# Kernel tuning notes

Hardware: AMD Instinct MI355X
Metric: run time of the kernel (lower is better)

The kernel has to match this reference:

```python
import jax, jax.numpy as jnp
import numpy as np

DIM = 768
NUM_HEADS = 12
HEAD_DIM = DIM // NUM_HEADS
SCALE = HEAD_DIM ** -0.5
NEG = -9e15


def setup_inputs() -> dict:
    key = jax.random.key(0)
    ks = jax.random.split(key, 8)
    B, N, M, C = 4, 1024, 2048, DIM
    q = jax.random.normal(ks[0], (B, N, C), dtype=jnp.float32)
    kv = jax.random.normal(ks[1], (B, M, C), dtype=jnp.float32)
    mask = jax.random.randint(ks[2], (B, 1, N, M), 0, 2, dtype=jnp.int32)
    s = 1.0 / np.sqrt(C)
    Wq = jax.random.normal(ks[3], (C, C), dtype=jnp.float32) * s      # nn.Linear(dim, dim), no bias
    Wkv = jax.random.normal(ks[4], (2 * C, C), dtype=jnp.float32) * s  # nn.Linear(dim, 2*dim), no bias
    Wproj = jax.random.normal(ks[5], (C, C), dtype=jnp.float32) * s
    bproj = jax.random.normal(ks[6], (C,), dtype=jnp.float32) * s
    return {"q": q, "kv": kv, "Wq": Wq, "Wkv": Wkv, "Wproj": Wproj, "bproj": bproj, "mask": mask}


def reference(q, kv, Wq, Wkv, Wproj, bproj, mask):
    B, M, C = kv.shape
    _, N, _ = q.shape
    H, d = NUM_HEADS, HEAD_DIM
    # kv projection -> [B, M, 2, H, d] -> k, v: [B, H, M, d]
    kvp = (kv @ Wkv.T).reshape(B, M, 2, H, d)
    k = kvp[:, :, 0].transpose(0, 2, 1, 3)
    v = kvp[:, :, 1].transpose(0, 2, 1, 3)
    # q projection -> [B, H, N, d], pre-scaled
    qp = (q @ Wq.T).reshape(B, N, H, d).transpose(0, 2, 1, 3) * SCALE
    attn = jnp.einsum('bhnd,bhmd->bhnm', qp, k)  # [B, H, N, M]
    attn = jnp.where(mask == 0, NEG, attn)
    attn = jax.nn.softmax(attn, axis=-1)
    # attn_drop / proj_drop have rate 0.0 (eval): identity
    x = jnp.einsum('bhnm,bhmd->bhnd', attn, v)
    x = x.transpose(0, 2, 1, 3).reshape(B, N, C)
    x = x @ Wproj.T + bproj
    return x
```

## Files before the change

kernel.cpp:

```cpp
#include <hip/hip_runtime.h>
#include <hip/hip_bf16.h>


typedef short    s16x8  __attribute__((ext_vector_type(8)));
typedef short    s16x4  __attribute__((ext_vector_type(4)));
typedef __bf16   bf16x8 __attribute__((ext_vector_type(8)));
typedef float    f32x4  __attribute__((ext_vector_type(4)));
typedef _Float16 f16x4  __attribute__((ext_vector_type(4)));
typedef _Float16 f16x2  __attribute__((ext_vector_type(2)));

#define NUM_H 12
#define DIM   768
#define NQ    1024
#define MK    2048
#define QK_SCALE_LOG2E 0.18033688f

__device__ __forceinline__ short f2b(float v) {
    __hip_bfloat16 h = __float2bfloat16(v);
    return __builtin_bit_cast(short, h);
}
__device__ __forceinline__ short f2h(float v) {
    _Float16 h = (_Float16)v;
    return __builtin_bit_cast(short, h);
}
__device__ __forceinline__ f32x4 mfma_bf16_k32(bf16x8 a, bf16x8 b, f32x4 c) {
    return __builtin_amdgcn_mfma_f32_16x16x32_bf16(a, b, c, 0, 0, 0);
}
__device__ __forceinline__ f32x4 mfma_f16_k16(f16x4 a, f16x4 b, f32x4 c) {
    return __builtin_amdgcn_mfma_f32_16x16x16f16(a, b, c, 0, 0, 0);
}
__device__ __forceinline__ f16x2 pk2h(float a, float b) {
    return __builtin_bit_cast(f16x2, __builtin_amdgcn_cvt_pkrtz(a, b));
}

__global__ __launch_bounds__(256) void prep_kernel(
    const float* __restrict__ q, const float* __restrict__ kv,
    const float* __restrict__ Wq, const float* __restrict__ Wkv,
    const float* __restrict__ Wp, const int* __restrict__ mask,
    short* __restrict__ q_bf, short* __restrict__ kv_bf,
    short* __restrict__ Wq_bf, short* __restrict__ Wkv_bf,
    short* __restrict__ Wp_bf, unsigned char* __restrict__ mbytes)
{
    int bid = blockIdx.x;
    if (bid < 5760) {
        const float* s; short* d; long base;
        if (bid < 1536)      { s = q;   d = q_bf;   base = (long)bid * 2048; }
        else if (bid < 4608) { s = kv;  d = kv_bf;  base = (long)(bid - 1536) * 2048; }
        else if (bid < 4896) { s = Wq;  d = Wq_bf;  base = (long)(bid - 4608) * 2048; }
        else if (bid < 5472) { s = Wkv; d = Wkv_bf; base = (long)(bid - 4896) * 2048; }
        else                 { s = Wp;  d = Wp_bf;  base = (long)(bid - 5472) * 2048; }
        long i = base + threadIdx.x * 8;
        float4 a = *(const float4*)(s + i);
        float4 b = *(const float4*)(s + i + 4);
        s16x8 r;
        r[0] = f2b(a.x); r[1] = f2b(a.y); r[2] = f2b(a.z); r[3] = f2b(a.w);
        r[4] = f2b(b.x); r[5] = f2b(b.y); r[6] = f2b(b.z); r[7] = f2b(b.w);
        *(s16x8*)(d + i) = r;
    } else {
        long base = (long)(bid - 5760) * 2048 + threadIdx.x * 8;
        int4 m0 = *(const int4*)(mask + base);
        int4 m1 = *(const int4*)(mask + base + 4);
        unsigned v = (unsigned)(m0.x != 0)        | ((unsigned)(m0.y != 0) << 1)
                   | ((unsigned)(m0.z != 0) << 2) | ((unsigned)(m0.w != 0) << 3)
                   | ((unsigned)(m1.x != 0) << 4) | ((unsigned)(m1.y != 0) << 5)
                   | ((unsigned)(m1.z != 0) << 6) | ((unsigned)(m1.w != 0) << 7);
        mbytes[base >> 3] = (unsigned char)v;
    }
}

__device__ __forceinline__ void gemm_core(
    short* smem,
    const short* __restrict__ A, const short* __restrict__ Bt,
    int Ncols, int mode, const float* __restrict__ bias,
    short* __restrict__ outb, short* __restrict__ outb2,
    float* __restrict__ outf, int bid)
{
    short (*As)[72] = (short(*)[72])smem;
    short (*Bs)[72] = (short(*)[72])(smem + 9216);

    int ntiles = Ncols >> 7;
    int m0 = (bid / ntiles) << 7;
    int n0 = (bid % ntiles) << 7;
    int t = threadIdx.x;
    int w = t >> 6, lane = t & 63, quad = lane >> 4, l16 = lane & 15;
    int wm = (w & 1) << 6, wn = (w >> 1) << 6;

    f32x4 zero4 = {0.f, 0.f, 0.f, 0.f};
    f32x4 acc[4][4];
    for (int i = 0; i < 4; i++)
        for (int j = 0; j < 4; j++) acc[i][j] = zero4;

    int lr = t >> 1;
    int lc = (t & 1) << 5;
    const short* Ap = A + (long)(m0 + lr) * DIM + lc;
    const short* Bp = Bt + (long)(n0 + lr) * DIM + lc;

    s16x8 a8[4], b8[4];
    #pragma unroll
    for (int c = 0; c < 4; c++) {
        a8[c] = *(const s16x8*)(Ap + c * 8);
        b8[c] = *(const s16x8*)(Bp + c * 8);
    }

    for (int kt = 0; kt < DIM; kt += 64) {
        __syncthreads();
        #pragma unroll
        for (int c = 0; c < 4; c++) {
            *(s16x8*)&As[lr][lc + c * 8] = a8[c];
            *(s16x8*)&Bs[lr][lc + c * 8] = b8[c];
        }
        __syncthreads();
        if (kt + 64 < DIM) {
            #pragma unroll
            for (int c = 0; c < 4; c++) {
                a8[c] = *(const s16x8*)(Ap + kt + 64 + c * 8);
                b8[c] = *(const s16x8*)(Bp + kt + 64 + c * 8);
            }
        }
        #pragma unroll
        for (int kh = 0; kh < 2; kh++) {
            bf16x8 af[4], bfr[4];
            #pragma unroll
            for (int i = 0; i < 4; i++) {
                s16x8 tmp = *(const s16x8*)&As[wm + i * 16 + l16][kh * 32 + quad * 8];
                af[i] = __builtin_bit_cast(bf16x8, tmp);
            }
            #pragma unroll
            for (int j = 0; j < 4; j++) {
                s16x8 tmp = *(const s16x8*)&Bs[wn + j * 16 + l16][kh * 32 + quad * 8];
                bfr[j] = __builtin_bit_cast(bf16x8, tmp);
            }
            #pragma unroll
            for (int i = 0; i < 4; i++)
                #pragma unroll
                for (int j = 0; j < 4; j++)
                    acc[i][j] = mfma_bf16_k32(af[i], bfr[j], acc[i][j]);
        }
    }

    __syncthreads();

    if (mode == 2) {
        #pragma unroll
        for (int i = 0; i < 4; i++)
            #pragma unroll
            for (int j = 0; j < 4; j++)
                #pragma unroll
                for (int r = 0; r < 4; r++) {
                    int row = m0 + wm + i * 16 + quad * 4 + r;
                    int col = n0 + wn + j * 16 + l16;
                    outf[(long)row * DIM + col] = acc[i][j][r] + bias[col];
                }
        return;
    }

    short (*Cs)[136] = (short(*)[136])smem;
    bool vreg = (mode == 1) && (n0 >= DIM);

    if (!vreg) {
        float sc = (mode == 0) ? QK_SCALE_LOG2E : 1.0f;
        #pragma unroll
        for (int i = 0; i < 4; i++)
            #pragma unroll
            for (int j = 0; j < 4; j++)
                #pragma unroll
                for (int r = 0; r < 4; r++)
                    Cs[wm + i * 16 + quad * 4 + r][wn + j * 16 + l16] =
                        f2b(acc[i][j][r] * sc);
    } else {
        #pragma unroll
        for (int i = 0; i < 4; i++)
            #pragma unroll
            for (int j = 0; j < 4; j++) {
                int c = wn + j * 16 + l16;
                int r0 = wm + i * 16 + quad * 4;
                s16x4 pk;
                pk[0] = f2h(acc[i][j][0]); pk[1] = f2h(acc[i][j][1]);
                pk[2] = f2h(acc[i][j][2]); pk[3] = f2h(acc[i][j][3]);
                *(s16x4*)&Cs[c][r0] = pk;
            }
    }
    __syncthreads();

    if (!vreg) {
        int hb2 = n0 >> 6;
        long rowsN = (mode == 0) ? NQ : MK;
        int b = (int)(m0 / rowsN);
        int rb = (int)(m0 % rowsN);
        short* ob0 = outb + ((long)(b * NUM_H + hb2) * rowsN + rb) * 64;
        short* ob1 = outb + ((long)(b * NUM_H + hb2 + 1) * rowsN + rb) * 64;
        #pragma unroll
        for (int k2 = 0; k2 < 8; k2++) {
            int ch = k2 * 256 + t;
            int half = ch >> 10, off = ch & 1023;
            s16x8 vd = *(const s16x8*)&Cs[off >> 3][(half << 6) + ((off & 7) << 3)];
            *(s16x8*)((half ? ob1 : ob0) + off * 8) = vd;
        }
    } else {
        int hb2 = (n0 - DIM) >> 6;
        int b = m0 >> 11, rb = m0 & 2047;
        #pragma unroll
        for (int k2 = 0; k2 < 8; k2++) {
            int ch = k2 * 256 + t;
            int c = ch >> 4, woff = (ch & 15) << 3;
            s16x8 vd = *(const s16x8*)&Cs[c][woff];
            int half = c >> 6, dd = c & 63;
            *(s16x8*)(outb2 + (((long)(b * NUM_H + hb2 + half) * 64 + dd) * MK + rb) + woff) = vd;
        }
    }
}

__global__ __launch_bounds__(256) void gemm12_kernel(
    const short* __restrict__ qbf, const short* __restrict__ Wqbf,
    const short* __restrict__ kvbf, const short* __restrict__ Wkvbf,
    short* __restrict__ qp, short* __restrict__ kk, short* __restrict__ vt)
{
    __shared__ short smem[18432];
    if (blockIdx.x < 192)
        gemm_core(smem, qbf, Wqbf, 768, 0, nullptr, qp, nullptr, nullptr, blockIdx.x);
    else
        gemm_core(smem, kvbf, Wkvbf, 1536, 1, nullptr, kk, vt, nullptr, blockIdx.x - 192);
}

__global__ __launch_bounds__(256) void gemm3_kernel(
    const short* __restrict__ xb, const short* __restrict__ Wpbf,
    const float* __restrict__ bias, float* __restrict__ out)
{
    __shared__ short smem[18432];
    gemm_core(smem, xb, Wpbf, 768, 2, bias, nullptr, nullptr, out, blockIdx.x);
}

__global__ __launch_bounds__(256) void attn_kernel(
    const short* __restrict__ qp, const short* __restrict__ kk,
    const short* __restrict__ vt, const unsigned* __restrict__ mb,
    short* __restrict__ xb)
{
    __shared__ short qs[64][72];
    __shared__ short ks[64][72];
    __shared__ short vs[64][72];

    int bid = blockIdx.x;
    int bh = bid % 48;
    int nt = bid / 48;
    int h = bh % NUM_H, b = bh / NUM_H;
    int n0 = nt << 6;
    int t = threadIdx.x, w = t >> 6, lane = t & 63, quad = lane >> 4, l16 = lane & 15;

    const short* qbase = qp + ((long)bh * NQ + n0) * 64;
    const short* kbase = kk + (long)bh * MK * 64;
    const short* vbase = vt + (long)bh * 64 * MK;
    const unsigned* mrow = mb + ((long)b * NQ + n0 + (w << 4) + l16) * 64;

    {
        int qr = t >> 2, c0 = (t & 3) << 4;
        *(s16x8*)&qs[qr][c0]     = *(const s16x8*)(qbase + qr * 64 + c0);
        *(s16x8*)&qs[qr][c0 + 8] = *(const s16x8*)(qbase + qr * 64 + c0 + 8);
    }
    __syncthreads();
    bf16x8 bq[2];
    {
        s16x8 t0 = *(const s16x8*)&qs[(w << 4) + l16][quad * 8];
        s16x8 t1 = *(const s16x8*)&qs[(w << 4) + l16][32 + quad * 8];
        bq[0] = __builtin_bit_cast(bf16x8, t0);
        bq[1] = __builtin_bit_cast(bf16x8, t1);
    }

    int sr = t >> 2, c0 = (t & 3) << 4;
    const short* kp = kbase + (long)sr * 64 + c0;
    const short* vp = vbase + (long)sr * MK + c0;

    s16x8 k0 = *(const s16x8*)(kp);
    s16x8 k1 = *(const s16x8*)(kp + 8);
    s16x8 v0 = *(const s16x8*)(vp);
    s16x8 v1 = *(const s16x8*)(vp + 8);
    uint2 mwv = *(const uint2*)(mrow);

    f32x4 zero4 = {0.f, 0.f, 0.f, 0.f};
    f32x4 o[4], ol = zero4;
    for (int j = 0; j < 4; j++) o[j] = zero4;
    const f16x4 ones = {(_Float16)1.f, (_Float16)1.f, (_Float16)1.f, (_Float16)1.f};

    for (int mt = 0; mt < MK; mt += 64) {
        __syncthreads();
        *(s16x8*)&ks[sr][c0]     = k0;
        *(s16x8*)&ks[sr][c0 + 8] = k1;
        *(s16x8*)&vs[sr][c0]     = v0;
        *(s16x8*)&vs[sr][c0 + 8] = v1;
        unsigned cm0 = mwv.x, cm1 = mwv.y;
        __syncthreads();
        if (mt + 64 < MK) {
            k0 = *(const s16x8*)(kp + (long)(mt + 64) * 64);
            k1 = *(const s16x8*)(kp + (long)(mt + 64) * 64 + 8);
            v0 = *(const s16x8*)(vp + mt + 64);
            v1 = *(const s16x8*)(vp + mt + 64 + 8);
            mwv = *(const uint2*)(mrow + ((mt + 64) >> 5));
        }

        f32x4 s[4];
        for (int j = 0; j < 4; j++) s[j] = zero4;
        #pragma unroll
        for (int kh = 0; kh < 2; kh++)
            #pragma unroll
            for (int j = 0; j < 4; j++) {
                s16x8 tk = *(const s16x8*)&ks[j * 16 + l16][kh * 32 + quad * 8];
                s[j] = mfma_bf16_k32(__builtin_bit_cast(bf16x8, tk), bq[kh], s[j]);
            }

        f16x4 pa[4];
        #pragma unroll
        for (int j = 0; j < 4; j++) {
            unsigned wsel = (j < 2) ? cm0 : cm1;
            unsigned bits = wsel >> (((j & 1) << 4) + (quad << 2));
            float p0 = (bits & 1u)        ? __builtin_amdgcn_exp2f(s[j][0]) : 0.f;
            float p1 = ((bits >> 1) & 1u) ? __builtin_amdgcn_exp2f(s[j][1]) : 0.f;
            float p2 = ((bits >> 2) & 1u) ? __builtin_amdgcn_exp2f(s[j][2]) : 0.f;
            float p3 = ((bits >> 3) & 1u) ? __builtin_amdgcn_exp2f(s[j][3]) : 0.f;
            f16x2 lo = pk2h(p0, p1);
            f16x2 hi = pk2h(p2, p3);
            pa[j] = __builtin_shufflevector(lo, hi, 0, 1, 2, 3);
        }

        #pragma unroll
        for (int j = 0; j < 4; j++) {
            ol = mfma_f16_k16(pa[j], ones, ol);
            #pragma unroll
            for (int jd = 0; jd < 4; jd++) {
                f16x4 bv = *(const f16x4*)&vs[jd * 16 + l16][j * 16 + quad * 4];
                o[jd] = mfma_f16_k16(pa[j], bv, o[jd]);
            }
        }
    }

    float linv[4];
    #pragma unroll
    for (int rr = 0; rr < 4; rr++) linv[rr] = 1.0f / ol[rr];
    short (*ps)[72] = (short(*)[72])&qs[w << 4];
    #pragma unroll
    for (int jd = 0; jd < 4; jd++)
        #pragma unroll
        for (int rr = 0; rr < 4; rr++)
            ps[quad * 4 + rr][jd * 16 + l16] = f2b(o[jd][rr] * linv[rr]);

    #pragma unroll
    for (int k2 = 0; k2 < 2; k2++) {
        int row = (lane >> 3) + k2 * 8;
        int cc = (lane & 7) << 3;
        s16x8 vd = *(const s16x8*)&ps[row][cc];
        *(s16x8*)(xb + ((long)b * NQ + n0 + (w << 4) + row) * DIM + h * 64 + cc) = vd;
    }
}

extern "C" void kernel_launch(void* const* d_in, const int* in_sizes, int n_in,
                              void* d_out, int out_size, void* d_ws, size_t ws_size,
                              hipStream_t stream)
{
    const float* q     = (const float*)d_in[0];
    const float* kv    = (const float*)d_in[1];
    const float* Wq    = (const float*)d_in[2];
    const float* Wkv   = (const float*)d_in[3];
    const float* Wproj = (const float*)d_in[4];
    const float* bproj = (const float*)d_in[5];
    const int*   mask  = (const int*)d_in[6];
    float* out = (float*)d_out;

    char* ws = (char*)d_ws;
    short* q_bf   = (short*)ws; ws += (size_t)4096 * 768 * 2;
    short* kv_bf  = (short*)ws; ws += (size_t)8192 * 768 * 2;
    short* Wq_bf  = (short*)ws; ws += (size_t)768 * 768 * 2;
    short* Wkv_bf = (short*)ws; ws += (size_t)1536 * 768 * 2;
    short* Wp_bf  = (short*)ws; ws += (size_t)768 * 768 * 2;
    short* qp     = (short*)ws; ws += (size_t)4096 * 768 * 2;
    short* kk     = (short*)ws; ws += (size_t)8192 * 768 * 2;
    short* vt     = (short*)ws; ws += (size_t)8192 * 768 * 2;
    short* xb     = (short*)ws; ws += (size_t)4096 * 768 * 2;
    unsigned char* mbytes = (unsigned char*)ws;

    prep_kernel<<<9856, 256, 0, stream>>>(q, kv, Wq, Wkv, Wproj, mask,
                                          q_bf, kv_bf, Wq_bf, Wkv_bf, Wp_bf, mbytes);
    gemm12_kernel<<<960, 256, 0, stream>>>(q_bf, Wq_bf, kv_bf, Wkv_bf, qp, kk, vt);
    attn_kernel<<<768, 256, 0, stream>>>(qp, kk, vt, (const unsigned*)mbytes, xb);
    gemm3_kernel<<<192, 256, 0, stream>>>(xb, Wp_bf, bproj, out);
}
```

Before: 221.7 us.

## Switch pipeline to fp16 and give each attention wave two query sub-tiles

All intermediate tensors and GEMMs now use fp16 instead of bf16, via the 16x16x32 f16 MFMA. The attention kernel drops to 128 threads per block, and each wave handles 32 query rows (two 16-row sub-tiles) that share one K/V LDS tile. Each loaded K fragment and V fragment then feeds two MFMAs, which cuts LDS reads per FLOP and lowers block-level sync overhead. The costs are higher register pressure, fewer waves per block to hide latency, and the narrower fp16 range for the projected activations, which skips the softmax max subtraction.

Result: slower. 226.5 us (+2.2%).

```diff
diff --git a/kernel.cpp b/kernel.cpp
--- a/kernel.cpp
+++ b/kernel.cpp
@@ -4,8 +4,8 @@
 
 typedef short    s16x8  __attribute__((ext_vector_type(8)));
 typedef short    s16x4  __attribute__((ext_vector_type(4)));
-typedef __bf16   bf16x8 __attribute__((ext_vector_type(8)));
 typedef float    f32x4  __attribute__((ext_vector_type(4)));
+typedef _Float16 f16x8  __attribute__((ext_vector_type(8)));
 typedef _Float16 f16x4  __attribute__((ext_vector_type(4)));
 typedef _Float16 f16x2  __attribute__((ext_vector_type(2)));
 
@@ -15,18 +15,14 @@
 #define MK    2048
 #define QK_SCALE_LOG2E 0.18033688f
 
-__device__ __forceinline__ short f2b(float v) {
-    __hip_bfloat16 h = __float2bfloat16(v);
-    return __builtin_bit_cast(short, h);
-}
 __device__ __forceinline__ short f2h(float v) {
     _Float16 h = (_Float16)v;
     return __builtin_bit_cast(short, h);
 }
-__device__ __forceinline__ f32x4 mfma_bf16_k32(bf16x8 a, bf16x8 b, f32x4 c) {
-    return __builtin_amdgcn_mfma_f32_16x16x32_bf16(a, b, c, 0, 0, 0);
-}
-__device__ __forceinline__ f32x4 mfma_f16_k16(f16x4 a, f16x4 b, f32x4 c) {
+__device__ __forceinline__ f32x4 mfma16x32(f16x8 a, f16x8 b, f32x4 c) {
+    return __builtin_amdgcn_mfma_f32_16x16x32_f16(a, b, c, 0, 0, 0);
+}
+__device__ __forceinline__ f32x4 mfma16x16(f16x4 a, f16x4 b, f32x4 c) {
     return __builtin_amdgcn_mfma_f32_16x16x16f16(a, b, c, 0, 0, 0);
 }
 __device__ __forceinline__ f16x2 pk2h(float a, float b) {
@@ -37,24 +33,24 @@
     const float* __restrict__ q, const float* __restrict__ kv,
     const float* __restrict__ Wq, const float* __restrict__ Wkv,
     const float* __restrict__ Wp, const int* __restrict__ mask,
-    short* __restrict__ q_bf, short* __restrict__ kv_bf,
-    short* __restrict__ Wq_bf, short* __restrict__ Wkv_bf,
-    short* __restrict__ Wp_bf, unsigned char* __restrict__ mbytes)
+    short* __restrict__ q_h, short* __restrict__ kv_h,
+    short* __restrict__ Wq_h, short* __restrict__ Wkv_h,
+    short* __restrict__ Wp_h, unsigned char* __restrict__ mbytes)
 {
     int bid = blockIdx.x;
     if (bid < 5760) {
         const float* s; short* d; long base;
-        if (bid < 1536)      { s = q;   d = q_bf;   base = (long)bid * 2048; }
-        else if (bid < 4608) { s = kv;  d = kv_bf;  base = (long)(bid - 1536) * 2048; }
-        else if (bid < 4896) { s = Wq;  d = Wq_bf;  base = (long)(bid - 4608) * 2048; }
-        else if (bid < 5472) { s = Wkv; d = Wkv_bf; base = (long)(bid - 4896) * 2048; }
-        else                 { s = Wp;  d = Wp_bf;  base = (long)(bid - 5472) * 2048; }
+        if (bid < 1536)      { s = q;   d = q_h;   base = (long)bid * 2048; }
+        else if (bid < 4608) { s = kv;  d = kv_h;  base = (long)(bid - 1536) * 2048; }
+        else if (bid < 4896) { s = Wq;  d = Wq_h;  base = (long)(bid - 4608) * 2048; }
+        else if (bid < 5472) { s = Wkv; d = Wkv_h; base = (long)(bid - 4896) * 2048; }
+        else                 { s = Wp;  d = Wp_h;  base = (long)(bid - 5472) * 2048; }
         long i = base + threadIdx.x * 8;
         float4 a = *(const float4*)(s + i);
         float4 b = *(const float4*)(s + i + 4);
         s16x8 r;
-        r[0] = f2b(a.x); r[1] = f2b(a.y); r[2] = f2b(a.z); r[3] = f2b(a.w);
-        r[4] = f2b(b.x); r[5] = f2b(b.y); r[6] = f2b(b.z); r[7] = f2b(b.w);
+        r[0] = f2h(a.x); r[1] = f2h(a.y); r[2] = f2h(a.z); r[3] = f2h(a.w);
+        r[4] = f2h(b.x); r[5] = f2h(b.y); r[6] = f2h(b.z); r[7] = f2h(b.w);
         *(s16x8*)(d + i) = r;
     } else {
         long base = (long)(bid - 5760) * 2048 + threadIdx.x * 8;
@@ -119,22 +115,22 @@
         }
         #pragma unroll
         for (int kh = 0; kh < 2; kh++) {
-            bf16x8 af[4], bfr[4];
+            f16x8 af[4], bfr[4];
             #pragma unroll
             for (int i = 0; i < 4; i++) {
                 s16x8 tmp = *(const s16x8*)&As[wm + i * 16 + l16][kh * 32 + quad * 8];
-                af[i] = __builtin_bit_cast(bf16x8, tmp);
+                af[i] = __builtin_bit_cast(f16x8, tmp);
             }
             #pragma unroll
             for (int j = 0; j < 4; j++) {
                 s16x8 tmp = *(const s16x8*)&Bs[wn + j * 16 + l16][kh * 32 + quad * 8];
-                bfr[j] = __builtin_bit_cast(bf16x8, tmp);
+                bfr[j] = __builtin_bit_cast(f16x8, tmp);
             }
             #pragma unroll
             for (int i = 0; i < 4; i++)
                 #pragma unroll
                 for (int j = 0; j < 4; j++)
-                    acc[i][j] = mfma_bf16_k32(af[i], bfr[j], acc[i][j]);
+                    acc[i][j] = mfma16x32(af[i], bfr[j], acc[i][j]);
         }
     }
 
@@ -166,7 +162,7 @@
                 #pragma unroll
                 for (int r = 0; r < 4; r++)
                     Cs[wm + i * 16 + quad * 4 + r][wn + j * 16 + l16] =
-                        f2b(acc[i][j][r] * sc);
+                        f2h(acc[i][j][r] * sc);
     } else {
         #pragma unroll
         for (int i = 0; i < 4; i++)
@@ -211,26 +207,26 @@
 }
 
 __global__ __launch_bounds__(256) void gemm12_kernel(
-    const short* __restrict__ qbf, const short* __restrict__ Wqbf,
-    const short* __restrict__ kvbf, const short* __restrict__ Wkvbf,
+    const short* __restrict__ qh, const short* __restrict__ Wqh,
+    const short* __restrict__ kvh, const short* __restrict__ Wkvh,
     short* __restrict__ qp, short* __restrict__ kk, short* __restrict__ vt)
 {
     __shared__ short smem[18432];
     if (blockIdx.x < 192)
-        gemm_core(smem, qbf, Wqbf, 768, 0, nullptr, qp, nullptr, nullptr, blockIdx.x);
+        gemm_core(smem, qh, Wqh, 768, 0, nullptr, qp, nullptr, nullptr, blockIdx.x);
     else
-        gemm_core(smem, kvbf, Wkvbf, 1536, 1, nullptr, kk, vt, nullptr, blockIdx.x - 192);
+        gemm_core(smem, kvh, Wkvh, 1536, 1, nullptr, kk, vt, nullptr, blockIdx.x - 192);
 }
 
 __global__ __launch_bounds__(256) void gemm3_kernel(
-    const short* __restrict__ xb, const short* __restrict__ Wpbf,
+    const short* __restrict__ xb, const short* __restrict__ Wph,
     const float* __restrict__ bias, float* __restrict__ out)
 {
     __shared__ short smem[18432];
-    gemm_core(smem, xb, Wpbf, 768, 2, bias, nullptr, nullptr, out, blockIdx.x);
-}
-
-__global__ __launch_bounds__(256) void attn_kernel(
+    gemm_core(smem, xb, Wph, 768, 2, bias, nullptr, nullptr, out, blockIdx.x);
+}
+
+__global__ __launch_bounds__(128) void attn_kernel(
     const short* __restrict__ qp, const short* __restrict__ kk,
     const short* __restrict__ vt, const unsigned* __restrict__ mb,
     short* __restrict__ xb)
@@ -249,104 +245,121 @@
     const short* qbase = qp + ((long)bh * NQ + n0) * 64;
     const short* kbase = kk + (long)bh * MK * 64;
     const short* vbase = vt + (long)bh * 64 * MK;
-    const unsigned* mrow = mb + ((long)b * NQ + n0 + (w << 4) + l16) * 64;
-
-    {
-        int qr = t >> 2, c0 = (t & 3) << 4;
-        *(s16x8*)&qs[qr][c0]     = *(const s16x8*)(qbase + qr * 64 + c0);
-        *(s16x8*)&qs[qr][c0 + 8] = *(const s16x8*)(qbase + qr * 64 + c0 + 8);
-    }
+    const unsigned* mrow0 = mb + ((long)b * NQ + n0 + (w << 5) + l16) * 64;
+    const unsigned* mrow1 = mrow0 + 16 * 64;
+
+    int gr = t >> 3, gc = (t & 7) << 3;
+    #pragma unroll
+    for (int i = 0; i < 4; i++)
+        *(s16x8*)&qs[gr + i * 16][gc] = *(const s16x8*)(qbase + (gr + i * 16) * 64 + gc);
     __syncthreads();
-    bf16x8 bq[2];
-    {
-        s16x8 t0 = *(const s16x8*)&qs[(w << 4) + l16][quad * 8];
-        s16x8 t1 = *(const s16x8*)&qs[(w << 4) + l16][32 + quad * 8];
-        bq[0] = __builtin_bit_cast(bf16x8, t0);
-        bq[1] = __builtin_bit_cast(bf16x8, t1);
-    }
-
-    int sr = t >> 2, c0 = (t & 3) << 4;
-    const short* kp = kbase + (long)sr * 64 + c0;
-    const short* vp = vbase + (long)sr * MK + c0;
-
-    s16x8 k0 = *(const s16x8*)(kp);
-    s16x8 k1 = *(const s16x8*)(kp + 8);
-    s16x8 v0 = *(const s16x8*)(vp);
-    s16x8 v1 = *(const s16x8*)(vp + 8);
-    uint2 mwv = *(const uint2*)(mrow);
+
+    f16x8 bq[2][2];
+    #pragma unroll
+    for (int s2 = 0; s2 < 2; s2++)
+        #pragma unroll
+        for (int kh = 0; kh < 2; kh++)
+            bq[s2][kh] = __builtin_bit_cast(f16x8,
+                *(const s16x8*)&qs[(w << 5) + (s2 << 4) + l16][kh * 32 + quad * 8]);
+
+    s16x8 k8[4], v8[4];
+    #pragma unroll
+    for (int i = 0; i < 4; i++) {
+        k8[i] = *(const s16x8*)(kbase + (long)(gr + i * 16) * 64 + gc);
+        v8[i] = *(const s16x8*)(vbase + (long)(gr + i * 16) * MK + gc);
+    }
+    uint2 mw0 = *(const uint2*)(mrow0);
+    uint2 mw1 = *(const uint2*)(mrow1);
 
     f32x4 zero4 = {0.f, 0.f, 0.f, 0.f};
-    f32x4 o[4], ol = zero4;
-    for (int j = 0; j < 4; j++) o[j] = zero4;
+    f32x4 o[2][4], ol[2];
+    #pragma unroll
+    for (int s2 = 0; s2 < 2; s2++) {
+        ol[s2] = zero4;
+        for (int j = 0; j < 4; j++) o[s2][j] = zero4;
+    }
     const f16x4 ones = {(_Float16)1.f, (_Float16)1.f, (_Float16)1.f, (_Float16)1.f};
 
     for (int mt = 0; mt < MK; mt += 64) {
         __syncthreads();
-        *(s16x8*)&ks[sr][c0]     = k0;
-        *(s16x8*)&ks[sr][c0 + 8] = k1;
-        *(s16x8*)&vs[sr][c0]     = v0;
-        *(s16x8*)&vs[sr][c0 + 8] = v1;
-        unsigned cm0 = mwv.x, cm1 = mwv.y;
+        #pragma unroll
+        for (int i = 0; i < 4; i++) {
+            *(s16x8*)&ks[gr + i * 16][gc] = k8[i];
+            *(s16x8*)&vs[gr + i * 16][gc] = v8[i];
+        }
+        unsigned cm[2][2] = {{mw0.x, mw0.y}, {mw1.x, mw1.y}};
         __syncthreads();
         if (mt + 64 < MK) {
-            k0 = *(const s16x8*)(kp + (long)(mt + 64) * 64);
-            k1 = *(const s16x8*)(kp + (long)(mt + 64) * 64 + 8);
-            v0 = *(const s16x8*)(vp + mt + 64);
-            v1 = *(const s16x8*)(vp + mt + 64 + 8);
-            mwv = *(const uint2*)(mrow + ((mt + 64) >> 5));
-        }
-
-        f32x4 s[4];
-        for (int j = 0; j < 4; j++) s[j] = zero4;
+            #pragma unroll
+            for (int i = 0; i < 4; i++) {
+                k8[i] = *(const s16x8*)(kbase + (long)(mt + 64 + gr + i * 16) * 64 + gc);
+                v8[i] = *(const s16x8*)(vbase + (long)(gr + i * 16) * MK + mt + 64 + gc);
+            }
+            mw0 = *(const uint2*)(mrow0 + ((mt + 64) >> 5));
+            mw1 = *(const uint2*)(mrow1 + ((mt + 64) >> 5));
+        }
+
+        f32x4 s[2][4];
+        #pragma unroll
+        for (int j = 0; j < 4; j++) { s[0][j] = zero4; s[1][j] = zero4; }
         #pragma unroll
         for (int kh = 0; kh < 2; kh++)
             #pragma unroll
             for (int j = 0; j < 4; j++) {
-                s16x8 tk = *(const s16x8*)&ks[j * 16 + l16][kh * 32 + quad * 8];
-                s[j] = mfma_bf16_k32(__builtin_bit_cast(bf16x8, tk), bq[kh], s[j]);
-            }
-
-        f16x4 pa[4];
+                f16x8 ak = __builtin_bit_cast(f16x8,
+                    *(const s16x8*)&ks[j * 16 + l16][kh * 32 + quad * 8]);
+                s[0][j] = mfma16x32(ak, bq[0][kh], s[0][j]);
+                s[1][j] = mfma16x32(ak, bq[1][kh], s[1][j]);
+            }
+
+        f16x4 pa[2][4];
+        #pragma unroll
+        for (int s2 = 0; s2 < 2; s2++)
+            #pragma unroll
+            for (int j = 0; j < 4; j++) {
+                unsigned wsel = (j < 2) ? cm[s2][0] : cm[s2][1];
+                unsigned bits = wsel >> (((j & 1) << 4) + (quad << 2));
+                float p0 = (bits & 1u)        ? __builtin_amdgcn_exp2f(s[s2][j][0]) : 0.f;
+                float p1 = ((bits >> 1) & 1u) ? __builtin_amdgcn_exp2f(s[s2][j][1]) : 0.f;
+                float p2 = ((bits >> 2) & 1u) ? __builtin_amdgcn_exp2f(s[s2][j][2]) : 0.f;
+                float p3 = ((bits >> 3) & 1u) ? __builtin_amdgcn_exp2f(s[s2][j][3]) : 0.f;
+                f16x2 lo = pk2h(p0, p1);
+                f16x2 hi = pk2h(p2, p3);
+                pa[s2][j] = __builtin_shufflevector(lo, hi, 0, 1, 2, 3);
+            }
+
         #pragma unroll
         for (int j = 0; j < 4; j++) {
-            unsigned wsel = (j < 2) ? cm0 : cm1;
-            unsigned bits = wsel >> (((j & 1) << 4) + (quad << 2));
-            float p0 = (bits & 1u)        ? __builtin_amdgcn_exp2f(s[j][0]) : 0.f;
-            float p1 = ((bits >> 1) & 1u) ? __builtin_amdgcn_exp2f(s[j][1]) : 0.f;
-            float p2 = ((bits >> 2) & 1u) ? __builtin_amdgcn_exp2f(s[j][2]) : 0.f;
-            float p3 = ((bits >> 3) & 1u) ? __builtin_amdgcn_exp2f(s[j][3]) : 0.f;
-            f16x2 lo = pk2h(p0, p1);
-            f16x2 hi = pk2h(p2, p3);
-            pa[j] = __builtin_shufflevector(lo, hi, 0, 1, 2, 3);
-        }
-
-        #pragma unroll
-        for (int j = 0; j < 4; j++) {
-            ol = mfma_f16_k16(pa[j], ones, ol);
+            ol[0] = mfma16x16(pa[0][j], ones, ol[0]);
+            ol[1] = mfma16x16(pa[1][j], ones, ol[1]);
             #pragma unroll
             for (int jd = 0; jd < 4; jd++) {
                 f16x4 bv = *(const f16x4*)&vs[jd * 16 + l16][j * 16 + quad * 4];
-                o[jd] = mfma_f16_k16(pa[j], bv, o[jd]);
-            }
-        }
-    }
-
-    float linv[4];
-    #pragma unroll
-    for (int rr = 0; rr < 4; rr++) linv[rr] = 1.0f / ol[rr];
-    short (*ps)[72] = (short(*)[72])&qs[w << 4];
-    #pragma unroll
-    for (int jd = 0; jd < 4; jd++)
-        #pragma unroll
-        for (int rr = 0; rr < 4; rr++)
-            ps[quad * 4 + rr][jd * 16 + l16] = f2b(o[jd][rr] * linv[rr]);
-
-    #pragma unroll
-    for (int k2 = 0; k2 < 2; k2++) {
-        int row = (lane >> 3) + k2 * 8;
+                o[0][jd] = mfma16x16(pa[0][j], bv, o[0][jd]);
+                o[1][jd] = mfma16x16(pa[1][j], bv, o[1][jd]);
+            }
+        }
+    }
+
+    #pragma unroll
+    for (int s2 = 0; s2 < 2; s2++) {
+        float linv[4];
+        #pragma unroll
+        for (int rr = 0; rr < 4; rr++) linv[rr] = 1.0f / ol[s2][rr];
+        #pragma unroll
+        for (int jd = 0; jd < 4; jd++)
+            #pragma unroll
+            for (int rr = 0; rr < 4; rr++)
+                qs[(w << 5) + (s2 << 4) + quad * 4 + rr][jd * 16 + l16] =
+                    f2h(o[s2][jd][rr] * linv[rr]);
+    }
+    __syncthreads();
+    #pragma unroll
+    for (int k2 = 0; k2 < 4; k2++) {
+        int row = (w << 5) + (lane >> 3) + k2 * 8;
         int cc = (lane & 7) << 3;
-        s16x8 vd = *(const s16x8*)&ps[row][cc];
-        *(s16x8*)(xb + ((long)b * NQ + n0 + (w << 4) + row) * DIM + h * 64 + cc) = vd;
+        s16x8 vd = *(const s16x8*)&qs[row][cc];
+        *(s16x8*)(xb + ((long)b * NQ + n0 + row) * DIM + h * 64 + cc) = vd;
     }
 }
 
@@ -364,20 +377,20 @@
     float* out = (float*)d_out;
 
     char* ws = (char*)d_ws;
-    short* q_bf   = (short*)ws; ws += (size_t)4096 * 768 * 2;
-    short* kv_bf  = (short*)ws; ws += (size_t)8192 * 768 * 2;
-    short* Wq_bf  = (short*)ws; ws += (size_t)768 * 768 * 2;
-    short* Wkv_bf = (short*)ws; ws += (size_t)1536 * 768 * 2;
-    short* Wp_bf  = (short*)ws; ws += (size_t)768 * 768 * 2;
-    short* qp     = (short*)ws; ws += (size_t)4096 * 768 * 2;
-    short* kk     = (short*)ws; ws += (size_t)8192 * 768 * 2;
-    short* vt     = (short*)ws; ws += (size_t)8192 * 768 * 2;
-    short* xb     = (short*)ws; ws += (size_t)4096 * 768 * 2;
+    short* q_h   = (short*)ws; ws += (size_t)4096 * 768 * 2;
+    short* kv_h  = (short*)ws; ws += (size_t)8192 * 768 * 2;
+    short* Wq_h  = (short*)ws; ws += (size_t)768 * 768 * 2;
+    short* Wkv_h = (short*)ws; ws += (size_t)1536 * 768 * 2;
+    short* Wp_h  = (short*)ws; ws += (size_t)768 * 768 * 2;
+    short* qp    = (short*)ws; ws += (size_t)4096 * 768 * 2;
+    short* kk    = (short*)ws; ws += (size_t)8192 * 768 * 2;
+    short* vt    = (short*)ws; ws += (size_t)8192 * 768 * 2;
+    short* xb    = (short*)ws; ws += (size_t)4096 * 768 * 2;
     unsigned char* mbytes = (unsigned char*)ws;
 
     prep_kernel<<<9856, 256, 0, stream>>>(q, kv, Wq, Wkv, Wproj, mask,
-                                          q_bf, kv_bf, Wq_bf, Wkv_bf, Wp_bf, mbytes);
-    gemm12_kernel<<<960, 256, 0, stream>>>(q_bf, Wq_bf, kv_bf, Wkv_bf, qp, kk, vt);
-    attn_kernel<<<768, 256, 0, stream>>>(qp, kk, vt, (const unsigned*)mbytes, xb);
-    gemm3_kernel<<<192, 256, 0, stream>>>(xb, Wp_bf, bproj, out);
-}
+                                          q_h, kv_h, Wq_h, Wkv_h, Wp_h, mbytes);
+    gemm12_kernel<<<960, 256, 0, stream>>>(q_h, Wq_h, kv_h, Wkv_h, qp, kk, vt);
+    attn_kernel<<<768, 128, 0, stream>>>(qp, kk, vt, (const unsigned*)mbytes, xb);
+    gemm3_kernel<<<192, 256, 0, stream>>>(xb, Wp_h, bproj, out);
+}
```
